# Performance work log

Hardware: AMD Instinct MI355X
Metric: run time of the kernel (lower is better)

The kernel has to match this reference:

```python
import jax, jax.numpy as jnp
import numpy as np

H_IMG, W_IMG = 256, 256
FX = FY = 300.0
CX, CY = W_IMG / 2.0, H_IMG / 2.0
NEAR, FAR = 0.01, 100.0
MAX_RADIUS = 64.0
N_GAUSS = 4096


def quat_to_rot(q):
    q = q / jnp.linalg.norm(q, axis=-1, keepdims=True)
    w, x, y, z = q[..., 0], q[..., 1], q[..., 2], q[..., 3]
    R = jnp.stack([
        1 - 2 * y * y - 2 * z * z, 2 * x * y - 2 * w * z, 2 * x * z + 2 * w * y,
        2 * x * y + 2 * w * z, 1 - 2 * x * x - 2 * z * z, 2 * y * z - 2 * w * x,
        2 * x * z - 2 * w * y, 2 * y * z + 2 * w * x, 1 - 2 * x * x - 2 * y * y,
    ], axis=-1)
    return R.reshape(q.shape[:-1] + (3, 3))


def setup_inputs():
    key = jax.random.key(0)
    k1, k2, k3, k4, k5, k6 = jax.random.split(key, 6)
    xy = jax.random.normal(k1, (N_GAUSS, 2), jnp.float32) * 2.0
    z = -(jax.random.uniform(k2, (N_GAUSS, 1), jnp.float32) * 6.0 + 2.0)  # depths in [2, 8]
    positions = jnp.concatenate([xy, z], axis=1)
    scales = jax.random.uniform(k3, (N_GAUSS, 3), jnp.float32) * 0.10 + 0.02
    rotations = jax.random.normal(k4, (N_GAUSS, 4), jnp.float32)
    colors = jax.random.uniform(k5, (N_GAUSS, 3), jnp.float32)
    opacities = jax.random.uniform(k6, (N_GAUSS,), jnp.float32) * 0.8 + 0.1
    view_matrix = jnp.eye(4, dtype=jnp.float32)
    return {"positions": positions, "scales": scales, "rotations": rotations,
            "colors": colors, "opacities": opacities, "view_matrix": view_matrix}


def _render(positions, scales, rotations, colors, opacities, view_matrix):
    N = positions.shape[0]
    pts = jnp.concatenate([positions, jnp.ones((N, 1), positions.dtype)], axis=1)
    pc = (view_matrix @ pts.T).T[:, :3]  # camera-space points (N,3)
    x, y, z = pc[:, 0], pc[:, 1], pc[:, 2]
    depths = -z
    z_safe = jnp.clip(jnp.abs(z), 0.01) * jnp.sign(z + 1e-8)
    z2 = z_safe * z_safe
    # 3D covariance = (Rcam R S)(Rcam R S)^T
    R = quat_to_rot(rotations)
    R_cam = view_matrix[:3, :3] @ R
    RS = R_cam * scales[:, None, :]  # right-multiply by diag(scales)
    cov3d = RS @ jnp.swapaxes(RS, -1, -2)
    # perspective Jacobian (N,2,3)
    zr = jnp.zeros_like(x)
    J = jnp.stack([
        jnp.stack([FX / -z_safe, zr, FX * x / z2], axis=-1),
        jnp.stack([zr, FY / z_safe, FY * y / z2], axis=-1),
    ], axis=-2)
    cov2d = J @ cov3d @ jnp.swapaxes(J, -1, -2)
    u = FX * x / -z_safe + CX
    v = FY * -y / -z_safe + CY
    # effective radius: 3 sigma from max eigenvalue of 2x2 covariance
    a, b = cov2d[:, 0, 0], cov2d[:, 0, 1]
    c, d = cov2d[:, 1, 0], cov2d[:, 1, 1]
    tr = a + d
    det = jnp.clip(a * d - b * c, 1e-6)
    disc = jnp.clip(tr * tr - 4.0 * det, 0.0)
    lam = (tr + jnp.sqrt(disc)) * 0.5
    radii = jnp.minimum(3.0 * jnp.sqrt(jnp.clip(lam, 1e-6)), MAX_RADIUS)
    # depth sort (front to back)
    order = jnp.argsort(depths)
    u, v, a, b, c, d = u[order], v[order], a[order], b[order], c[order], d[order]
    radii, depths = radii[order], depths[order]
    colors_s, op_s = colors[order], opacities[order]
    # visibility culling: zero opacity instead of compaction (same math, static shapes)
    visible = (depths > NEAR) & (depths < FAR)
    visible &= (u + radii > 0) & (u - radii < W_IMG)
    visible &= (v + radii > 0) & (v - radii < H_IMG)
    op_s = jnp.where(visible, op_s, 0.0)
    # regularized 2x2 inverse (pinv of PD matrix == inverse)
    ar, dr = a + 1e-4, d + 1e-4
    inv_det = 1.0 / (ar * dr - b * c)
    ia, ib, ic, idd = dr * inv_det, -b * inv_det, -c * inv_det, ar * inv_det
    px = jnp.arange(W_IMG, dtype=jnp.float32)[None, :]
    py = jnp.arange(H_IMG, dtype=jnp.float32)[:, None]

    def step(carry, g):
        acc_c, acc_a = carry
        mx, my, gia, gib, gic, gid, r, col, o = g
        dx = px - mx  # (1,W)
        dy = py - my  # (H,1)
        power = -0.5 * (gia * dx * dx + (gib + gic) * dx * dy + gid * dy * dy)
        # bounding-box mask replicating the torch tile bounds [int(m-r), int(m+r)+1)
        inside = ((px >= jnp.trunc(mx - r)) & (px <= jnp.trunc(mx + r))
                  & (py >= jnp.trunc(my - r)) & (py <= jnp.trunc(my + r)))
        alpha = jnp.where(inside, o * jnp.exp(power), 0.0)
        w = alpha * (1.0 - acc_a)  # front-to-back over-compositing
        return (acc_c + w[..., None] * col, acc_a + w), None

    acc0 = (jnp.zeros((H_IMG, W_IMG, 3), jnp.float32),
            jnp.zeros((H_IMG, W_IMG), jnp.float32))
    (acc_c, acc_a), _ = jax.lax.scan(
        step, acc0, (u, v, ia, ib, ic, idd, radii, colors_s, op_s))
    bg = jnp.zeros(3, jnp.float32)
    img = acc_c + (1.0 - acc_a)[..., None] * bg
    return jnp.transpose(img, (2, 0, 1))  # (3,H,W)


def reference(positions, scales, rotations, colors, opacities, view_matrix):
    return _render(positions, scales, rotations, colors, opacities, view_matrix)
```

## Files before the change

kernel.cpp:

```cpp
#include <hip/hip_runtime.h>
#include <hip/hip_fp16.h>
#include <math.h>

#define N_G   4096
#define CAP   1024
#define W_IMG 256
#define H_IMG 256

__global__ __launch_bounds__(64) void prep(
    const float* __restrict__ pos, const float* __restrict__ scl,
    const float* __restrict__ rot, const float* __restrict__ col,
    const float* __restrict__ opa, const float* __restrict__ vm,
    float4* __restrict__ gaussU, short4* __restrict__ bbhU,
    float* __restrict__ depthU)
{
  const int i = blockIdx.x * 64 + threadIdx.x;
  if (i >= N_G) return;
  const float FX=300.f, FY=300.f, CXc=128.f, CYc=128.f;
  const float HLOG2E = 0.72134752f;
  float V00=vm[0],V01=vm[1],V02=vm[2],V03=vm[3];
  float V10=vm[4],V11=vm[5],V12=vm[6],V13=vm[7];
  float V20=vm[8],V21=vm[9],V22=vm[10],V23=vm[11];
  float p0=pos[3*i], p1=pos[3*i+1], p2=pos[3*i+2];
  float X = V00*p0+V01*p1+V02*p2+V03;
  float Y = V10*p0+V11*p1+V12*p2+V13;
  float Z = V20*p0+V21*p1+V22*p2+V23;
  float depth = -Z;
  float zp = Z + 1e-8f;
  float sgn = (zp>0.f)?1.f:((zp<0.f)?-1.f:0.f);
  float z_safe = fmaxf(fabsf(Z), 0.01f) * sgn;
  float z2 = z_safe*z_safe;
  float qw=rot[4*i], qx=rot[4*i+1], qy=rot[4*i+2], qz=rot[4*i+3];
  float qi = 1.f/sqrtf(qw*qw+qx*qx+qy*qy+qz*qz);
  qw*=qi; qx*=qi; qy*=qi; qz*=qi;
  float R00=1.f-2.f*qy*qy-2.f*qz*qz, R01=2.f*qx*qy-2.f*qw*qz, R02=2.f*qx*qz+2.f*qw*qy;
  float R10=2.f*qx*qy+2.f*qw*qz, R11=1.f-2.f*qx*qx-2.f*qz*qz, R12=2.f*qy*qz-2.f*qw*qx;
  float R20=2.f*qx*qz-2.f*qw*qy, R21=2.f*qy*qz+2.f*qw*qx, R22=1.f-2.f*qx*qx-2.f*qy*qy;
  float C00=V00*R00+V01*R10+V02*R20, C01=V00*R01+V01*R11+V02*R21, C02=V00*R02+V01*R12+V02*R22;
  float C10=V10*R00+V11*R10+V12*R20, C11=V10*R01+V11*R11+V12*R21, C12=V10*R02+V11*R12+V12*R22;
  float C20=V20*R00+V21*R10+V22*R20, C21=V20*R01+V21*R11+V22*R21, C22=V20*R02+V21*R12+V22*R22;
  float s0=scl[3*i], s1=scl[3*i+1], s2=scl[3*i+2];
  float S00=C00*s0,S01=C01*s1,S02=C02*s2;
  float S10=C10*s0,S11=C11*s1,S12=C12*s2;
  float S20=C20*s0,S21=C21*s1,S22=C22*s2;
  float c00=S00*S00+S01*S01+S02*S02;
  float c01=S00*S10+S01*S11+S02*S12;
  float c02=S00*S20+S01*S21+S02*S22;
  float c11=S10*S10+S11*S11+S12*S12;
  float c12=S10*S20+S11*S21+S12*S22;
  float c22=S20*S20+S21*S21+S22*S22;
  float j00=FX/(-z_safe), j02=FX*X/z2;
  float j11=FY/z_safe,    j12=FY*Y/z2;
  float M00=j00*c00+j02*c02, M01=j00*c01+j02*c12, M02=j00*c02+j02*c22;
  float M10=j11*c01+j12*c02, M11=j11*c11+j12*c12, M12=j11*c12+j12*c22;
  float a =M00*j00+M02*j02;
  float b =M01*j11+M02*j12;
  float c_=M10*j00+M12*j02;
  float d =M11*j11+M12*j12;
  float u = FX*X/(-z_safe)+CXc;
  float v = FY*(-Y)/(-z_safe)+CYc;
  float tr=a+d;
  float det=fmaxf(a*d-b*c_, 1e-6f);
  float disc=fmaxf(tr*tr-4.f*det, 0.f);
  float lam=(tr+sqrtf(disc))*0.5f;
  float radius=fminf(3.f*sqrtf(fmaxf(lam,1e-6f)), 64.f);
  bool vis = (depth>0.01f)&&(depth<100.f)
          && (u+radius>0.f)&&(u-radius<(float)W_IMG)
          && (v+radius>0.f)&&(v-radius<(float)H_IMG);
  float o = vis ? opa[i] : 0.f;
  float ar=a+1e-4f, dr=d+1e-4f;
  float inv=1.f/(ar*dr-b*c_);
  short4 bb = make_short4(1000, -1000, 1000, -1000);
  if (o>0.f) {
    bb.x=(short)truncf(u-radius); bb.y=(short)truncf(u+radius);
    bb.z=(short)truncf(v-radius); bb.w=(short)truncf(v+radius);
  }
  unsigned hrg = (unsigned)__half_as_ushort(__float2half_rn(col[3*i]))
               | ((unsigned)__half_as_ushort(__float2half_rn(col[3*i+1]))<<16);
  depthU[i] = depth;
  bbhU[i]   = bb;
  gaussU[2*i]   = make_float4(u, v, (dr*inv)*HLOG2E,
                              ((-b*inv)+(-c_*inv))*HLOG2E);
  gaussU[2*i+1] = make_float4((ar*inv)*HLOG2E, log2f(o),
                              __uint_as_float(hrg), col[3*i+2]);
}

__global__ __launch_bounds__(1024) void render(
    const short4* __restrict__ bbhU, const float4* __restrict__ gaussU,
    const float* __restrict__ depthU, float* __restrict__ out)
{
  __shared__ __align__(16) unsigned long long keys[CAP];
  __shared__ float4 gp[CAP*2];
  __shared__ short4 bbh[CAP];
  __shared__ float4 res[16][64];
  __shared__ int lcnt;

  const int tid = threadIdx.x, wv = tid>>6, lane = tid&63;
  const int bid = (int)((blockIdx.x * 331u) & 511u);
  const int RX0=(bid&15)*16, RY0=(bid>>4)*8;
  const int RX1=RX0+15, RY1=RY0+7;

  if (tid==0) lcnt=0;
  __syncthreads();

  {
    short4 bb[4];
    #pragma unroll
    for (int c4=0;c4<4;c4++) bb[c4]=bbhU[(wv*4+c4)*64+lane];
    #pragma unroll
    for (int c4=0;c4<4;c4++) {
      int idx=(wv*4+c4)*64+lane;
      bool pred=(bb[c4].y>=RX0)&&(bb[c4].x<=RX1)&&(bb[c4].w>=RY0)&&(bb[c4].z<=RY1);
      unsigned long long m=__ballot(pred);
      if (m) {
        int bse=0;
        if (lane==0) bse=atomicAdd(&lcnt, __popcll(m));
        bse=__shfl(bse,0);
        if (pred) {
          int p=bse+__popcll(m&((1ull<<lane)-1ull));
          if (p<CAP)
            keys[p]=((unsigned long long)__float_as_uint(depthU[idx])<<12)
                   |(unsigned)idx;
        }
      }
    }
  }
  __syncthreads();
  const int len = (lcnt<CAP)?lcnt:CAP;

  if (tid<len) {
    unsigned long long kj=keys[tid];
    int r=0;
    const ulonglong2* k2=(const ulonglong2*)keys;
    int n2=len>>1;
    for(int s2=0;s2<n2;s2++){
      ulonglong2 kv=k2[s2];
      r += (kv.x<kj)+(kv.y<kj);
    }
    if(len&1) r += (keys[len-1]<kj);
    int idx=(int)(kj&4095u);
    gp[2*r]  =gaussU[2*idx];
    gp[2*r+1]=gaussU[2*idx+1];
    bbh[r]   =bbhU[idx];
  }
  __syncthreads();

  const int t=wv>>3, seg=wv&7;
  const int TX0=RX0+t*8, TY0=RY0, TX1=TX0+7, TY1=TY0+7;
  const int ipx=TX0+(lane&7), ipy=TY0+(lane>>3);
  const float px=(float)ipx, py=(float)ipy;
  const int segLen=(len+7)>>3;
  const int s=seg*segLen;
  int e=s+segLen; if(e>len) e=len;
  float aR=0.f,aG=0.f,aB=0.f,aA=0.f;
  for(int k0=s;k0<e;k0+=64){
    int kk=k0+lane;
    bool ok=false;
    if(kk<e){
      short4 bb=bbh[kk];
      ok=(bb.y>=TX0)&&(bb.x<=TX1)&&(bb.w>=TY0)&&(bb.z<=TY1);
    }
    unsigned long long mm=__ballot(ok);
    if(mm){
      int k=k0+__builtin_ctzll(mm); mm&=mm-1;
      short4 bb=bbh[k];
      float4 A=gp[2*k], B=gp[2*k+1];
      while(mm){
        int kn=k0+__builtin_ctzll(mm); mm&=mm-1;
        short4 bbn=bbh[kn];
        float4 An=gp[2*kn], Bn=gp[2*kn+1];
        float dx=px-A.x, dy=py-A.y;
        float q2=A.z*dx*dx + A.w*dx*dy + B.x*dy*dy;
        bool inside=(ipx>=bb.x)&&(ipx<=bb.y)&&(ipy>=bb.z)&&(ipy<=bb.w);
        float ex=__builtin_amdgcn_exp2f(B.y-q2);
        float alpha= inside ? ex : 0.f;
        float w=alpha*(1.f-aA);
        unsigned hrg=__float_as_uint(B.z);
        float cR=__half2float(__ushort_as_half((unsigned short)(hrg&0xFFFFu)));
        float cG=__half2float(__ushort_as_half((unsigned short)(hrg>>16)));
        aR+=w*cR; aG+=w*cG; aB+=w*B.w; aA+=w;
        bb=bbn; A=An; B=Bn;
      }
      float dx=px-A.x, dy=py-A.y;
      float q2=A.z*dx*dx + A.w*dx*dy + B.x*dy*dy;
      bool inside=(ipx>=bb.x)&&(ipx<=bb.y)&&(ipy>=bb.z)&&(ipy<=bb.w);
      float ex=__builtin_amdgcn_exp2f(B.y-q2);
      float alpha= inside ? ex : 0.f;
      float w=alpha*(1.f-aA);
      unsigned hrg=__float_as_uint(B.z);
      float cR=__half2float(__ushort_as_half((unsigned short)(hrg&0xFFFFu)));
      float cG=__half2float(__ushort_as_half((unsigned short)(hrg>>16)));
      aR+=w*cR; aG+=w*cG; aB+=w*B.w; aA+=w;
    }
    if(__ballot(aA<=0.9999f)==0ull) break;
  }
  res[wv][lane]=make_float4(aR,aG,aB,aA);
  __syncthreads();

  if(seg==0){
    float4 P=res[wv][lane];
    #pragma unroll
    for(int w=1;w<8;w++){
      float4 Q=res[wv+w][lane];
      float tr_=1.f-P.w;
      P.x+=tr_*Q.x; P.y+=tr_*Q.y; P.z+=tr_*Q.z; P.w+=tr_*Q.w;
    }
    out[0*H_IMG*W_IMG + ipy*W_IMG + ipx]=P.x;
    out[1*H_IMG*W_IMG + ipy*W_IMG + ipx]=P.y;
    out[2*H_IMG*W_IMG + ipy*W_IMG + ipx]=P.z;
  }
}

extern "C" void kernel_launch(void* const* d_in, const int* in_sizes, int n_in,
                              void* d_out, int out_size, void* d_ws, size_t ws_size,
                              hipStream_t stream)
{
  const float* pos=(const float*)d_in[0];
  const float* scl=(const float*)d_in[1];
  const float* rot=(const float*)d_in[2];
  const float* col=(const float*)d_in[3];
  const float* opa=(const float*)d_in[4];
  const float* vm =(const float*)d_in[5];
  float* out=(float*)d_out;
  char* ws=(char*)d_ws;
  float4* gaussU=(float4*)(ws);
  short4* bbhU  =(short4*)(ws + 128*1024);
  float*  depthU=(float*) (ws + 160*1024);
  prep<<<N_G/64, 64, 0, stream>>>(pos,scl,rot,col,opa,vm,gaussU,bbhU,depthU);
  render<<<512, 1024, 0, stream>>>(bbhU,gaussU,depthU,out);
}
```

Measured before the change: 19.31 us.

## Split rank-sort across two thread halves and pack bbox and fp32 color into gaussian record

When a block's candidate list holds at most 512 entries, the counting-sort rank computation is divided between both halves of the 1024-thread block, each scanning half of the keys, and partial ranks are combined through the reused shared result buffer. The gather is also split so each half copies different parts of the record. The gaussian record grows from two to three float4s, storing colors as full fp32 and the bounding box as packed 16-bit ints, so the separate bbox shared array and the fp16 color unpacking are gone. This adds an extra barrier and more shared-memory traffic per gaussian in the render loop, and in exchange shortens the serial sort phase.

```diff
diff --git a/kernel.cpp b/kernel.cpp
--- a/kernel.cpp
+++ b/kernel.cpp
@@ -75,14 +75,16 @@
     bb.x=(short)truncf(u-radius); bb.y=(short)truncf(u+radius);
     bb.z=(short)truncf(v-radius); bb.w=(short)truncf(v+radius);
   }
-  unsigned hrg = (unsigned)__half_as_ushort(__float2half_rn(col[3*i]))
-               | ((unsigned)__half_as_ushort(__float2half_rn(col[3*i+1]))<<16);
+  int bxy = ((int)bb.x & 0xFFFF) | ((int)bb.y << 16);
+  int bzw = ((int)bb.z & 0xFFFF) | ((int)bb.w << 16);
   depthU[i] = depth;
   bbhU[i]   = bb;
-  gaussU[2*i]   = make_float4(u, v, (dr*inv)*HLOG2E,
+  gaussU[3*i]   = make_float4(u, v, (dr*inv)*HLOG2E,
                               ((-b*inv)+(-c_*inv))*HLOG2E);
-  gaussU[2*i+1] = make_float4((ar*inv)*HLOG2E, log2f(o),
-                              __uint_as_float(hrg), col[3*i+2]);
+  gaussU[3*i+1] = make_float4((ar*inv)*HLOG2E, log2f(o),
+                              col[3*i], col[3*i+1]);
+  gaussU[3*i+2] = make_float4(col[3*i+2], __int_as_float(bxy),
+                              __int_as_float(bzw), 0.f);
 }
 
 __global__ __launch_bounds__(1024) void render(
@@ -90,10 +92,10 @@
     const float* __restrict__ depthU, float* __restrict__ out)
 {
   __shared__ __align__(16) unsigned long long keys[CAP];
-  __shared__ float4 gp[CAP*2];
-  __shared__ short4 bbh[CAP];
+  __shared__ float4 gp[CAP*3];
   __shared__ float4 res[16][64];
   __shared__ int lcnt;
+  int* pr = (int*)res;
 
   const int tid = threadIdx.x, wv = tid>>6, lane = tid&63;
   const int bid = (int)((blockIdx.x * 331u) & 511u);
@@ -127,21 +129,57 @@
   }
   __syncthreads();
   const int len = (lcnt<CAP)?lcnt:CAP;
-
-  if (tid<len) {
-    unsigned long long kj=keys[tid];
-    int r=0;
+  const bool split = (len <= 512);
+
+  if (split) {
     const ulonglong2* k2=(const ulonglong2*)keys;
-    int n2=len>>1;
-    for(int s2=0;s2<n2;s2++){
-      ulonglong2 kv=k2[s2];
-      r += (kv.x<kj)+(kv.y<kj);
-    }
-    if(len&1) r += (keys[len-1]<kj);
-    int idx=(int)(kj&4095u);
-    gp[2*r]  =gaussU[2*idx];
-    gp[2*r+1]=gaussU[2*idx+1];
-    bbh[r]   =bbhU[idx];
+    int n2=len>>1, nA=n2>>1;
+    if (tid < len) {
+      unsigned long long kj=keys[tid];
+      int r=0;
+      for(int s2=0;s2<nA;s2++){ ulonglong2 kv=k2[s2]; r+=(kv.x<kj)+(kv.y<kj); }
+      pr[tid]=r;
+    } else if (tid-512 < len) {
+      int j=tid-512;
+      unsigned long long kj=keys[j];
+      int r=0;
+      for(int s2=nA;s2<n2;s2++){ ulonglong2 kv=k2[s2]; r+=(kv.x<kj)+(kv.y<kj); }
+      if(len&1) r += (keys[len-1]<kj);
+      pr[tid]=r;
+    }
+  } else {
+    if (tid < len) {
+      unsigned long long kj=keys[tid];
+      const ulonglong2* k2=(const ulonglong2*)keys;
+      int n2=len>>1;
+      int r=0;
+      for(int s2=0;s2<n2;s2++){ ulonglong2 kv=k2[s2]; r+=(kv.x<kj)+(kv.y<kj); }
+      if(len&1) r += (keys[len-1]<kj);
+      pr[tid]=r;
+    }
+  }
+  __syncthreads();
+
+  if (split) {
+    if (tid < len) {
+      int r=pr[tid]+pr[512+tid];
+      int idx=(int)(keys[tid]&4095u);
+      gp[3*r]  =gaussU[3*idx];
+      gp[3*r+1]=gaussU[3*idx+1];
+    } else if (tid-512 < len) {
+      int j=tid-512;
+      int r=pr[j]+pr[tid];
+      int idx=(int)(keys[j]&4095u);
+      gp[3*r+2]=gaussU[3*idx+2];
+    }
+  } else {
+    if (tid < len) {
+      int r=pr[tid];
+      int idx=(int)(keys[tid]&4095u);
+      gp[3*r]  =gaussU[3*idx];
+      gp[3*r+1]=gaussU[3*idx+1];
+      gp[3*r+2]=gaussU[3*idx+2];
+    }
   }
   __syncthreads();
 
@@ -157,40 +195,38 @@
     int kk=k0+lane;
     bool ok=false;
     if(kk<e){
-      short4 bb=bbh[kk];
-      ok=(bb.y>=TX0)&&(bb.x<=TX1)&&(bb.w>=TY0)&&(bb.z<=TY1);
+      float4 Ck=gp[3*kk+2];
+      int bxy=__float_as_int(Ck.y), bzw=__float_as_int(Ck.z);
+      int Lx=(bxy<<16)>>16, Ux=bxy>>16, Ly=(bzw<<16)>>16, Uy=bzw>>16;
+      ok=(Ux>=TX0)&&(Lx<=TX1)&&(Uy>=TY0)&&(Ly<=TY1);
     }
     unsigned long long mm=__ballot(ok);
     if(mm){
       int k=k0+__builtin_ctzll(mm); mm&=mm-1;
-      short4 bb=bbh[k];
-      float4 A=gp[2*k], B=gp[2*k+1];
+      float4 A=gp[3*k], B=gp[3*k+1], C=gp[3*k+2];
       while(mm){
         int kn=k0+__builtin_ctzll(mm); mm&=mm-1;
-        short4 bbn=bbh[kn];
-        float4 An=gp[2*kn], Bn=gp[2*kn+1];
+        float4 An=gp[3*kn], Bn=gp[3*kn+1], Cn=gp[3*kn+2];
+        int bxy=__float_as_int(C.y), bzw=__float_as_int(C.z);
+        int Lx=(bxy<<16)>>16, Ux=bxy>>16, Ly=(bzw<<16)>>16, Uy=bzw>>16;
         float dx=px-A.x, dy=py-A.y;
         float q2=A.z*dx*dx + A.w*dx*dy + B.x*dy*dy;
-        bool inside=(ipx>=bb.x)&&(ipx<=bb.y)&&(ipy>=bb.z)&&(ipy<=bb.w);
+        bool inside=(ipx>=Lx)&&(ipx<=Ux)&&(ipy>=Ly)&&(ipy<=Uy);
         float ex=__builtin_amdgcn_exp2f(B.y-q2);
         float alpha= inside ? ex : 0.f;
         float w=alpha*(1.f-aA);
-        unsigned hrg=__float_as_uint(B.z);
-        float cR=__half2float(__ushort_as_half((unsigned short)(hrg&0xFFFFu)));
-        float cG=__half2float(__ushort_as_half((unsigned short)(hrg>>16)));
-        aR+=w*cR; aG+=w*cG; aB+=w*B.w; aA+=w;
-        bb=bbn; A=An; B=Bn;
+        aR+=w*B.z; aG+=w*B.w; aB+=w*C.x; aA+=w;
+        A=An; B=Bn; C=Cn;
       }
+      int bxy=__float_as_int(C.y), bzw=__float_as_int(C.z);
+      int Lx=(bxy<<16)>>16, Ux=bxy>>16, Ly=(bzw<<16)>>16, Uy=bzw>>16;
       float dx=px-A.x, dy=py-A.y;
       float q2=A.z*dx*dx + A.w*dx*dy + B.x*dy*dy;
-      bool inside=(ipx>=bb.x)&&(ipx<=bb.y)&&(ipy>=bb.z)&&(ipy<=bb.w);
+      bool inside=(ipx>=Lx)&&(ipx<=Ux)&&(ipy>=Ly)&&(ipy<=Uy);
       float ex=__builtin_amdgcn_exp2f(B.y-q2);
       float alpha= inside ? ex : 0.f;
       float w=alpha*(1.f-aA);
-      unsigned hrg=__float_as_uint(B.z);
-      float cR=__half2float(__ushort_as_half((unsigned short)(hrg&0xFFFFu)));
-      float cG=__half2float(__ushort_as_half((unsigned short)(hrg>>16)));
-      aR+=w*cR; aG+=w*cG; aB+=w*B.w; aA+=w;
+      aR+=w*B.z; aG+=w*B.w; aB+=w*C.x; aA+=w;
     }
     if(__ballot(aA<=0.9999f)==0ull) break;
   }
@@ -224,8 +260,8 @@
   float* out=(float*)d_out;
   char* ws=(char*)d_ws;
   float4* gaussU=(float4*)(ws);
-  short4* bbhU  =(short4*)(ws + 128*1024);
-  float*  depthU=(float*) (ws + 160*1024);
+  short4* bbhU  =(short4*)(ws + 192*1024);
+  float*  depthU=(float*) (ws + 224*1024);
   prep<<<N_G/64, 64, 0, stream>>>(pos,scl,rot,col,opa,vm,gaussU,bbhU,depthU);
   render<<<512, 1024, 0, stream>>>(bbhU,gaussU,depthU,out);
 }
```

Result: slower. 20.30 us (+5.1%).
